# Kernel tuning notes

Measured on AMD Instinct MI355X. Metric: run time of the kernel, lower is better.

The kernel has to match this reference:

```python
import jax, jax.numpy as jnp
import numpy as np

ST_RATIO = 1.5  # slice-thickness / in-plane-resolution ratio (module init arg)


def setup_inputs() -> dict:
    key = jax.random.key(0)
    k1, k2 = jax.random.split(key)
    B, H, W, D, S = 8, 160, 160, 96, 64
    vol = jax.random.normal(k1, (B, H, W, D, 1), dtype=jnp.float32)
    # small perturbations around identity (identity row is added inside reference)
    trf = jax.random.normal(k2, (B, S, 12), dtype=jnp.float32) * 0.05
    return {"vol": vol, "trf": trf}


def _trilinear(v, loc):
    """v: [H, W, D] volume; loc: [..., 3] float sample locations (voxel coords).
    Border-clipped trilinear interpolation (as in neuron's interpn)."""
    H, W, D = v.shape
    maxs_f = jnp.asarray([H - 1, W - 1, D - 1], dtype=loc.dtype)
    loc = jnp.clip(loc, 0.0, maxs_f)
    f = jnp.floor(loc)
    d = loc - f  # fractional part, in [0, 1)
    i0 = f.astype(jnp.int32)
    i1 = jnp.minimum(i0 + 1, jnp.asarray([H - 1, W - 1, D - 1], dtype=jnp.int32))
    out = jnp.zeros(loc.shape[:-1], dtype=v.dtype)
    for cx in (0, 1):
        for cy in (0, 1):
            for cz in (0, 1):
                ix = i1[..., 0] if cx else i0[..., 0]
                iy = i1[..., 1] if cy else i0[..., 1]
                iz = i1[..., 2] if cz else i0[..., 2]
                w = ((d[..., 0] if cx else 1.0 - d[..., 0])
                     * (d[..., 1] if cy else 1.0 - d[..., 1])
                     * (d[..., 2] if cz else 1.0 - d[..., 2]))
                out = out + w * v[ix, iy, iz]
    return out


def reference(vol, trf):
    """Volume-to-slice resampling.
    vol: [B, H, W, D, 1]; trf: [B, S, 12] per-slice affine params (flattened 3x4).
    Identity row added per original: trf += eye(4)[:3, :].
    Output: [B, H, W, S, 1]."""
    B, H, W, D, _ = vol.shape
    S = trf.shape[1]
    A = trf.reshape(B, S, 3, 4) + jnp.eye(4, dtype=trf.dtype)[:3, :]  # [B,S,3,4]

    # slice-plane sampling grid: in-plane (i, j) over HxW, through-plane z = s * st_ratio
    ii, jj = jnp.meshgrid(jnp.arange(H, dtype=jnp.float32),
                          jnp.arange(W, dtype=jnp.float32), indexing="ij")
    zz = jnp.arange(S, dtype=jnp.float32) * ST_RATIO
    ones = jnp.ones((S, H, W), dtype=jnp.float32)
    grid = jnp.stack([ii[None] * ones, jj[None] * ones,
                      zz[:, None, None] * ones, ones], axis=-1)  # [S,H,W,4] homogeneous

    loc = jnp.einsum("bsij,shwj->bshwi", A, grid)  # [B,S,H,W,3] volume coords
    out = jax.vmap(_trilinear)(vol[..., 0], loc)    # [B,S,H,W]
    return jnp.transpose(out, (0, 2, 3, 1))[..., None]  # [B,H,W,S,1]
```

## Files before the change

kernel.cpp:

```cpp
#include <hip/hip_runtime.h>
#include <hip/hip_fp16.h>

#define B 8
#define H 160
#define W 160
#define D 96
#define S 64
#define ST_RATIO 1.5f

__global__ __launch_bounds__(256) void v2s_prep3(
    const float* __restrict__ vol, __half2* __restrict__ volP)
{
    __shared__ __half ph[D * 164];
    const int bh = blockIdx.x;
    const float* in = vol + (size_t)bh * (W * D);

    for (int i = threadIdx.x; i < W * (D / 4); i += 256) {
        const int w_ = i / 24, k = i - w_ * 24;
        const float4 f = *(const float4*)(in + w_ * D + 4 * k);
        const int d0 = 4 * k;
        ph[(d0 + 0) * 164 + w_] = __float2half(f.x);
        ph[(d0 + 1) * 164 + w_] = __float2half(f.y);
        ph[(d0 + 2) * 164 + w_] = __float2half(f.z);
        ph[(d0 + 3) * 164 + w_] = __float2half(f.w);
    }
    __syncthreads();

    __half2* op = volP + (size_t)bh * (D * W);
    for (int i = threadIdx.x; i < D * (W / 4); i += 256) {
        const int d = i / 40, g = i - d * 40;
        const int w0 = 4 * g;
        const __half* row = &ph[d * 164];
        const ushort4 a = *(const ushort4*)(row + w0);
        const unsigned a4 = (unsigned)__half_as_ushort(row[min(w0 + 4, W - 1)]);
        int4 o;
        o.x = (int)((unsigned)a.x | ((unsigned)a.y << 16));
        o.y = (int)((unsigned)a.y | ((unsigned)a.z << 16));
        o.z = (int)((unsigned)a.z | ((unsigned)a.w << 16));
        o.w = (int)((unsigned)a.w | (a4 << 16));
        *(int4*)(op + (size_t)d * W + w0) = o;
    }
}

__global__ __launch_bounds__(256) void v2s_main4(
    const __half2* __restrict__ volP,
    const float*   __restrict__ trf,
    float*         __restrict__ out)
{
    __shared__ float As[S * 12];
    __shared__ float outT[64][65];

    const int bid  = blockIdx.x;
    const int tile = (bid & 7) * 400 + (bid >> 3);
    const int b    = tile / 400;
    const int hw0  = (tile - b * 400) * 64;

    const float* tb = trf + (size_t)b * (S * 12);
    for (int e = threadIdx.x; e < S * 12; e += 256) {
        const int j = e % 12;
        float v = tb[e];
        if ((j & 3) == (j >> 2)) v += 1.0f;
        As[e] = v;
    }
    __syncthreads();

    const int lane = threadIdx.x & 63;
    const int wid  = threadIdx.x >> 6;
    const int hw   = hw0 + lane;
    const int h    = hw / W;
    const int w    = hw - h * W;
    const float fh = (float)h, fw = (float)w;
    const __half2* vb = volP + (size_t)b * (H * D * W);

#pragma unroll 4
    for (int it = 0; it < 16; ++it) {
        const int s = it * 4 + wid;
        const float* a = &As[s * 12];
        const float fz = (float)s * ST_RATIO;

        float x = fmaf(a[0], fh, fmaf(a[1], fw, fmaf(a[2],  fz, a[3])));
        float y = fmaf(a[4], fh, fmaf(a[5], fw, fmaf(a[6],  fz, a[7])));
        float z = fmaf(a[8], fh, fmaf(a[9], fw, fmaf(a[10], fz, a[11])));

        x = fminf(fmaxf(x, 0.0f), (float)(H - 1));
        y = fminf(fmaxf(y, 0.0f), (float)(W - 1));
        z = fminf(fmaxf(z, 0.0f), (float)(D - 1));

        const float flx = floorf(x), fly = floorf(y), flz = floorf(z);
        const float dx = x - flx, dy = y - fly, dz = z - flz;
        const int ix0 = (int)flx, iy0 = (int)fly, iz0 = (int)flz;
        const int ix1 = min(ix0 + 1, H - 1);
        const int iz1 = min(iz0 + 1, D - 1);

        const int r0 = ix0 * D, r1 = ix1 * D;
        const float2 l00 = __half22float2(vb[(r0 + iz0) * W + iy0]);
        const float2 l01 = __half22float2(vb[(r0 + iz1) * W + iy0]);
        const float2 l10 = __half22float2(vb[(r1 + iz0) * W + iy0]);
        const float2 l11 = __half22float2(vb[(r1 + iz1) * W + iy0]);

        const float c00 = fmaf(dy, l00.y - l00.x, l00.x);
        const float c01 = fmaf(dy, l01.y - l01.x, l01.x);
        const float c10 = fmaf(dy, l10.y - l10.x, l10.x);
        const float c11 = fmaf(dy, l11.y - l11.x, l11.x);
        const float c0  = fmaf(dz, c01 - c00, c00);
        const float c1  = fmaf(dz, c11 - c10, c10);
        outT[lane][s]   = fmaf(dx, c1 - c0, c0);
    }
    __syncthreads();

    const int s_out = lane;
#pragma unroll
    for (int r = 0; r < 16; ++r) {
        const int hw_off = wid + 4 * r;
        out[((size_t)(b * (H * W) + hw0 + hw_off)) * S + s_out] = outT[hw_off][s_out];
    }
}

__global__ __launch_bounds__(256) void v2s_fallback(
    const float* __restrict__ vol, const float* __restrict__ trf,
    float* __restrict__ out)
{
    __shared__ float As[S * 13];
    const int pos0 = blockIdx.x * 4;
    const int b = pos0 / (H * W);
    const float* tb = trf + (size_t)b * S * 12;
    for (int e = threadIdx.x; e < S * 12; e += 256) {
        int s = e / 12, j = e - s * 12;
        float v = tb[e];
        if ((j & 3) == (j >> 2)) v += 1.0f;
        As[s * 13 + j] = v;
    }
    __syncthreads();
    const int s   = threadIdx.x & 63;
    const int pos = pos0 + (threadIdx.x >> 6);
    const int hw  = pos % (H * W);
    const int h   = hw / W;
    const int w   = hw - h * W;
    const float* a = &As[s * 13];
    const float fh = (float)h, fw = (float)w, fz = (float)s * ST_RATIO;
    float x = fmaf(a[0], fh, fmaf(a[1], fw, fmaf(a[2],  fz, a[3])));
    float y = fmaf(a[4], fh, fmaf(a[5], fw, fmaf(a[6],  fz, a[7])));
    float z = fmaf(a[8], fh, fmaf(a[9], fw, fmaf(a[10], fz, a[11])));
    x = fminf(fmaxf(x, 0.0f), (float)(H - 1));
    y = fminf(fmaxf(y, 0.0f), (float)(W - 1));
    z = fminf(fmaxf(z, 0.0f), (float)(D - 1));
    const float flx = floorf(x), fly = floorf(y), flz = floorf(z);
    const float dx = x - flx, dy = y - fly, dz = z - flz;
    const int ix0 = (int)flx, iy0 = (int)fly, iz0 = (int)flz;
    const int ix1 = min(ix0 + 1, H - 1);
    const int iy1 = min(iy0 + 1, W - 1);
    const int iz1 = min(iz0 + 1, D - 1);
    const float* vb  = vol + (size_t)b * (H * W * D);
    const float* p00 = vb + (ix0 * W + iy0) * D;
    const float* p01 = vb + (ix0 * W + iy1) * D;
    const float* p10 = vb + (ix1 * W + iy0) * D;
    const float* p11 = vb + (ix1 * W + iy1) * D;
    const float v000 = p00[iz0], v001 = p00[iz1];
    const float v010 = p01[iz0], v011 = p01[iz1];
    const float v100 = p10[iz0], v101 = p10[iz1];
    const float v110 = p11[iz0], v111 = p11[iz1];
    const float c00 = fmaf(dz, v001 - v000, v000);
    const float c01 = fmaf(dz, v011 - v010, v010);
    const float c10 = fmaf(dz, v101 - v100, v100);
    const float c11 = fmaf(dz, v111 - v110, v110);
    const float c0  = fmaf(dy, c01 - c00, c00);
    const float c1  = fmaf(dy, c11 - c10, c10);
    out[(size_t)pos * S + s] = fmaf(dx, c1 - c0, c0);
}

extern "C" void kernel_launch(void* const* d_in, const int* in_sizes, int n_in,
                              void* d_out, int out_size, void* d_ws, size_t ws_size,
                              hipStream_t stream) {
    const float* vol = (const float*)d_in[0];
    const float* trf = (const float*)d_in[1];
    float* out = (float*)d_out;

    const size_t volP_bytes = (size_t)B * H * D * W * sizeof(__half2);
    if (ws_size >= volP_bytes) {
        __half2* volP = (__half2*)d_ws;
        v2s_prep3<<<B * H, 256, 0, stream>>>(vol, volP);
        v2s_main4<<<3200, 256, 0, stream>>>(volP, trf, out);
    } else {
        v2s_fallback<<<(B * H * W) / 4, 256, 0, stream>>>(vol, trf, out);
    }
}
```

Baseline: 175.2 us.

## Split prep kernel across W halves and software-pipeline gather loads in main kernel

The prep kernel now splits each (b,h) row into two W-halves of 80 columns, using a smaller shared buffer and twice as many blocks, which should raise occupancy and parallelism. The main kernel is restructured into a software pipeline: the next slice's coordinate math and four half2 gathers are issued before the current slice is interpolated, with the loop fully unrolled. This is meant to hide gather latency, at the cost of extra register pressure.

Result: no change. 174.8 us (-0.2%).

```diff
diff --git a/kernel.cpp b/kernel.cpp
--- a/kernel.cpp
+++ b/kernel.cpp
@@ -8,31 +8,34 @@
 #define S 64
 #define ST_RATIO 1.5f
 
-__global__ __launch_bounds__(256) void v2s_prep3(
+__global__ __launch_bounds__(256) void v2s_prep4(
     const float* __restrict__ vol, __half2* __restrict__ volP)
 {
-    __shared__ __half ph[D * 164];
-    const int bh = blockIdx.x;
+    __shared__ __half ph[D * 84];
+    const int blk   = blockIdx.x;
+    const int bh    = blk >> 1;
+    const int wbase = (blk & 1) * 80;
     const float* in = vol + (size_t)bh * (W * D);
 
-    for (int i = threadIdx.x; i < W * (D / 4); i += 256) {
-        const int w_ = i / 24, k = i - w_ * 24;
+    for (int i = threadIdx.x; i < 81 * (D / 4); i += 256) {
+        const int rr = i / 24, k = i - rr * 24;
+        const int w_ = min(wbase + rr, W - 1);
         const float4 f = *(const float4*)(in + w_ * D + 4 * k);
         const int d0 = 4 * k;
-        ph[(d0 + 0) * 164 + w_] = __float2half(f.x);
-        ph[(d0 + 1) * 164 + w_] = __float2half(f.y);
-        ph[(d0 + 2) * 164 + w_] = __float2half(f.z);
-        ph[(d0 + 3) * 164 + w_] = __float2half(f.w);
-    }
-    __syncthreads();
-
-    __half2* op = volP + (size_t)bh * (D * W);
-    for (int i = threadIdx.x; i < D * (W / 4); i += 256) {
-        const int d = i / 40, g = i - d * 40;
+        ph[(d0 + 0) * 84 + rr] = __float2half(f.x);
+        ph[(d0 + 1) * 84 + rr] = __float2half(f.y);
+        ph[(d0 + 2) * 84 + rr] = __float2half(f.z);
+        ph[(d0 + 3) * 84 + rr] = __float2half(f.w);
+    }
+    __syncthreads();
+
+    __half2* op = volP + (size_t)bh * (D * W) + wbase;
+    for (int i = threadIdx.x; i < D * 20; i += 256) {
+        const int d = i / 20, g = i - d * 20;
         const int w0 = 4 * g;
-        const __half* row = &ph[d * 164];
+        const __half* row = &ph[d * 84];
         const ushort4 a = *(const ushort4*)(row + w0);
-        const unsigned a4 = (unsigned)__half_as_ushort(row[min(w0 + 4, W - 1)]);
+        const unsigned a4 = (unsigned)__half_as_ushort(row[w0 + 4]);
         int4 o;
         o.x = (int)((unsigned)a.x | ((unsigned)a.y << 16));
         o.y = (int)((unsigned)a.y | ((unsigned)a.z << 16));
@@ -42,7 +45,42 @@
     }
 }
 
-__global__ __launch_bounds__(256) void v2s_main4(
+struct Pk {
+    float dx, dy, dz;
+    __half2 v00, v01, v10, v11;
+};
+
+__device__ __forceinline__ Pk v2s_issue(
+    const float* __restrict__ As, int s, float fh, float fw,
+    const __half2* __restrict__ vb)
+{
+    const float* a = &As[s * 12];
+    const float fz = (float)s * ST_RATIO;
+
+    float x = fmaf(a[0], fh, fmaf(a[1], fw, fmaf(a[2],  fz, a[3])));
+    float y = fmaf(a[4], fh, fmaf(a[5], fw, fmaf(a[6],  fz, a[7])));
+    float z = fmaf(a[8], fh, fmaf(a[9], fw, fmaf(a[10], fz, a[11])));
+
+    x = fminf(fmaxf(x, 0.0f), (float)(H - 1));
+    y = fminf(fmaxf(y, 0.0f), (float)(W - 1));
+    z = fminf(fmaxf(z, 0.0f), (float)(D - 1));
+
+    const float flx = floorf(x), fly = floorf(y), flz = floorf(z);
+    const int ix0 = (int)flx, iy0 = (int)fly, iz0 = (int)flz;
+    const int ix1 = min(ix0 + 1, H - 1);
+    const int iz1 = min(iz0 + 1, D - 1);
+    const int r0 = ix0 * D, r1 = ix1 * D;
+
+    Pk p;
+    p.dx = x - flx; p.dy = y - fly; p.dz = z - flz;
+    p.v00 = vb[(r0 + iz0) * W + iy0];
+    p.v01 = vb[(r0 + iz1) * W + iy0];
+    p.v10 = vb[(r1 + iz0) * W + iy0];
+    p.v11 = vb[(r1 + iz1) * W + iy0];
+    return p;
+}
+
+__global__ __launch_bounds__(256) void v2s_main5(
     const __half2* __restrict__ volP,
     const float*   __restrict__ trf,
     float*         __restrict__ out)
@@ -72,39 +110,25 @@
     const float fh = (float)h, fw = (float)w;
     const __half2* vb = volP + (size_t)b * (H * D * W);
 
-#pragma unroll 4
+    Pk cur = v2s_issue(As, wid, fh, fw, vb);
+#pragma unroll
     for (int it = 0; it < 16; ++it) {
-        const int s = it * 4 + wid;
-        const float* a = &As[s * 12];
-        const float fz = (float)s * ST_RATIO;
-
-        float x = fmaf(a[0], fh, fmaf(a[1], fw, fmaf(a[2],  fz, a[3])));
-        float y = fmaf(a[4], fh, fmaf(a[5], fw, fmaf(a[6],  fz, a[7])));
-        float z = fmaf(a[8], fh, fmaf(a[9], fw, fmaf(a[10], fz, a[11])));
-
-        x = fminf(fmaxf(x, 0.0f), (float)(H - 1));
-        y = fminf(fmaxf(y, 0.0f), (float)(W - 1));
-        z = fminf(fmaxf(z, 0.0f), (float)(D - 1));
-
-        const float flx = floorf(x), fly = floorf(y), flz = floorf(z);
-        const float dx = x - flx, dy = y - fly, dz = z - flz;
-        const int ix0 = (int)flx, iy0 = (int)fly, iz0 = (int)flz;
-        const int ix1 = min(ix0 + 1, H - 1);
-        const int iz1 = min(iz0 + 1, D - 1);
-
-        const int r0 = ix0 * D, r1 = ix1 * D;
-        const float2 l00 = __half22float2(vb[(r0 + iz0) * W + iy0]);
-        const float2 l01 = __half22float2(vb[(r0 + iz1) * W + iy0]);
-        const float2 l10 = __half22float2(vb[(r1 + iz0) * W + iy0]);
-        const float2 l11 = __half22float2(vb[(r1 + iz1) * W + iy0]);
-
-        const float c00 = fmaf(dy, l00.y - l00.x, l00.x);
-        const float c01 = fmaf(dy, l01.y - l01.x, l01.x);
-        const float c10 = fmaf(dy, l10.y - l10.x, l10.x);
-        const float c11 = fmaf(dy, l11.y - l11.x, l11.x);
-        const float c0  = fmaf(dz, c01 - c00, c00);
-        const float c1  = fmaf(dz, c11 - c10, c10);
-        outT[lane][s]   = fmaf(dx, c1 - c0, c0);
+        Pk nxt;
+        if (it < 15) nxt = v2s_issue(As, (it + 1) * 4 + wid, fh, fw, vb);
+
+        const float2 l00 = __half22float2(cur.v00);
+        const float2 l01 = __half22float2(cur.v01);
+        const float2 l10 = __half22float2(cur.v10);
+        const float2 l11 = __half22float2(cur.v11);
+        const float c00 = fmaf(cur.dy, l00.y - l00.x, l00.x);
+        const float c01 = fmaf(cur.dy, l01.y - l01.x, l01.x);
+        const float c10 = fmaf(cur.dy, l10.y - l10.x, l10.x);
+        const float c11 = fmaf(cur.dy, l11.y - l11.x, l11.x);
+        const float c0  = fmaf(cur.dz, c01 - c00, c00);
+        const float c1  = fmaf(cur.dz, c11 - c10, c10);
+        outT[lane][it * 4 + wid] = fmaf(cur.dx, c1 - c0, c0);
+
+        cur = nxt;
     }
     __syncthreads();
 
@@ -178,8 +202,8 @@
     const size_t volP_bytes = (size_t)B * H * D * W * sizeof(__half2);
     if (ws_size >= volP_bytes) {
         __half2* volP = (__half2*)d_ws;
-        v2s_prep3<<<B * H, 256, 0, stream>>>(vol, volP);
-        v2s_main4<<<3200, 256, 0, stream>>>(volP, trf, out);
+        v2s_prep4<<<B * H * 2, 256, 0, stream>>>(vol, volP);
+        v2s_main5<<<3200, 256, 0, stream>>>(volP, trf, out);
     } else {
         v2s_fallback<<<(B * H * W) / 4, 256, 0, stream>>>(vol, trf, out);
     }
```
